# Performance work log

Hardware: AMD Instinct MI355X
Metric: run time of the kernel (lower is better)

Reference implementation:

```python
import jax, jax.numpy as jnp
import numpy as np

C = 256
DEPTH = 4
GRIDS = [(128, 128), (128, 128), (128, 128)]
B = 2
N = 32768


def _ln_c(x, g, b):
    # LayerNorm over channel dim of [B, C, N] (myLayerNorm transposes to [B,N,C])
    m = x.mean(axis=1, keepdims=True)
    v = ((x - m) ** 2).mean(axis=1, keepdims=True)
    return (x - m) * jax.lax.rsqrt(v + 1e-5) * g[None, :, None] + b[None, :, None]


def _bn_train(x, g, b):
    # BatchNorm1d (training-mode batch stats) over [B, C, L]
    m = x.mean(axis=(0, 2), keepdims=True)
    v = ((x - m) ** 2).mean(axis=(0, 2), keepdims=True)
    return (x - m) * jax.lax.rsqrt(v + 1e-5) * g[None, :, None] + b[None, :, None]


def _dwconv3(x, w, b):
    # depthwise 3x3 conv, SAME padding; x [B,C,H,W], w [C,3,3]
    out = jax.lax.conv_general_dilated(x, w[:, None, :, :], (1, 1), 'SAME',
                                       feature_group_count=C,
                                       dimension_numbers=('NCHW', 'OIHW', 'NCHW'))
    return out + b[None, :, None, None]


def setup_inputs() -> dict:
    key = jax.random.key(0)
    ks = jax.random.split(key, 20)
    tokens = jax.random.normal(ks[0], (B, C, N), jnp.float32)
    hw = GRIDS[0][0] * GRIDS[0][1]
    cell_ind = jax.random.randint(ks[1], (B, 3, N), 0, hw)
    occupied_cell = jnp.ones((B, N), jnp.float32)

    def p(k, shape, scale=0.05):
        return scale * jax.random.normal(k, shape, jnp.float32)

    inp = dict(tokens=tokens, cell_ind=cell_ind, occupied_cell=occupied_cell)
    inp['smix_ln_g'] = 1.0 + p(ks[2], (DEPTH, C))
    inp['smix_ln_b'] = p(ks[3], (DEPTH, C))
    inp['ffn_w1'] = p(ks[4], (DEPTH, C, 3, 3), 0.2)
    inp['ffn_b1'] = p(ks[5], (DEPTH, C))
    inp['ffn_w2'] = p(ks[6], (DEPTH, C, 3, 3), 0.2)
    inp['ffn_b2'] = p(ks[7], (DEPTH, C))
    inp['att_scale'] = 1.0 + p(ks[8], (DEPTH, C))
    inp['att_bn_g'] = 1.0 + p(ks[9], (DEPTH, C))
    inp['att_bn_b'] = p(ks[10], (DEPTH, C))
    inp['cmix_ln_g'] = 1.0 + p(ks[11], (DEPTH, C))
    inp['cmix_ln_b'] = p(ks[12], (DEPTH, C))
    inp['cmix_w1'] = p(ks[13], (DEPTH, C, C), 1.0 / float(np.sqrt(C)))
    inp['cmix_b1'] = p(ks[14], (DEPTH, C))
    inp['cmix_w2'] = p(ks[15], (DEPTH, C, C), 1.0 / float(np.sqrt(C)))
    inp['cmix_b2'] = p(ks[16], (DEPTH, C))
    inp['cmix_scale'] = p(ks[17], (DEPTH, C), 0.1)
    return inp


def _forward(tokens, occupied_cell, cell_ind,
             smix_ln_g, smix_ln_b, ffn_w1, ffn_b1, ffn_w2, ffn_b2,
             att_scale, att_bn_g, att_bn_b,
             cmix_ln_g, cmix_ln_b, cmix_w1, cmix_b1, cmix_w2, cmix_b2, cmix_scale):
    Bx, Cx, Nx = tokens.shape
    bidx = jnp.arange(Bx)[:, None]
    # build_proj_matrix equivalent: per-point 1/(points-in-cell) weights + clamped indices
    sp = []
    for g in range(len(GRIDS)):
        HW = GRIDS[g][0] * GRIDS[g][1]
        ci = jnp.clip(cell_ind[:, g], 0, HW - 1)
        # inflate^T @ occupied: per-cell occupied count (occupied^2 per point)
        counts = jnp.zeros((Bx, HW), tokens.dtype).at[bidx, ci].add(occupied_cell * occupied_cell)
        # inflate @ counts: per-point count of points sharing its cell
        npp = occupied_cell * jnp.take_along_axis(counts, ci, axis=1)
        sp.append((ci, occupied_cell / (npp + 1e-6)))
    skip = [jnp.zeros(GRIDS[g], tokens.dtype) for g in range(len(GRIDS))]
    for d in range(DEPTH):
        g = d % len(GRIDS)
        H, W = GRIDS[g]
        HW = H * W
        ci, wpt = sp[g]
        # --- SpatialMix ---
        r = _ln_c(tokens, smix_ln_g[d], smix_ln_b[d]) * wpt[:, None, :]
        grid = jnp.zeros((Bx, Cx, HW), tokens.dtype).at[
            jnp.arange(Bx)[:, None, None], jnp.arange(Cx)[None, :, None], ci[:, None, :]].add(r)
        grid = grid.reshape(Bx, Cx, H, W) + skip[g]
        plane = _dwconv3(jax.nn.relu(_dwconv3(grid, ffn_w1[d], ffn_b1[d])), ffn_w2[d], ffn_b2[d])
        rflat = plane.reshape(Bx, Cx, HW)
        att = jax.nn.sigmoid(_bn_train(rflat * att_scale[d][None, :, None], att_bn_g[d], att_bn_b[d]))
        rflat = att * rflat
        r = jnp.take_along_axis(rflat, jnp.broadcast_to(ci[:, None, :], (Bx, Cx, Nx)), axis=2)
        tokens = tokens + r
        skip[g] = plane
        # --- ChannelMix ---
        h = _ln_c(tokens, cmix_ln_g[d], cmix_ln_b[d])
        h = jnp.einsum('oc,bcn->bon', cmix_w1[d], h) + cmix_b1[d][None, :, None]
        h = jnp.einsum('oc,bcn->bon', cmix_w2[d], jax.nn.relu(h)) + cmix_b2[d][None, :, None]
        tokens = tokens + h * cmix_scale[d][None, :, None]
    return tokens


def reference(tokens, cell_ind, occupied_cell,
              smix_ln_g, smix_ln_b, ffn_w1, ffn_b1, ffn_w2, ffn_b2,
              att_scale, att_bn_g, att_bn_b,
              cmix_ln_g, cmix_ln_b, cmix_w1, cmix_b1, cmix_w2, cmix_b2, cmix_scale):
    return _forward(tokens, occupied_cell, cell_ind,
                    smix_ln_g, smix_ln_b, ffn_w1, ffn_b1, ffn_w2, ffn_b2,
                    att_scale, att_bn_g, att_bn_b,
                    cmix_ln_g, cmix_ln_b, cmix_w1, cmix_b1, cmix_w2, cmix_b2, cmix_scale)
```

## Files before the change

kernel.cpp:

```cpp
#include <hip/hip_runtime.h>
#include <hip/hip_bf16.h>
#include <hip/hip_fp16.h>

#define Cc 256
#define Nn 32768
#define HWc 16384
#define Bb 2

typedef float floatx4 __attribute__((ext_vector_type(4)));
typedef short bf16x8 __attribute__((ext_vector_type(8)));
typedef unsigned short ushort8v __attribute__((ext_vector_type(8)));
typedef unsigned short ushort4v __attribute__((ext_vector_type(4)));

__device__ __forceinline__ unsigned short f2b(float f){
    unsigned u = __float_as_uint(f);
    u += 0x7fff + ((u >> 16) & 1);
    return (unsigned short)(u >> 16);
}
__device__ __forceinline__ float b2f(unsigned short h){
    return __uint_as_float(((unsigned)h) << 16);
}
__device__ __forceinline__ unsigned short f2h(float f){
    return __half_as_ushort(__float2half(f));
}
__device__ __forceinline__ float h2f(unsigned short h){
    return __half2float(__ushort_as_half(h));
}

__global__ __launch_bounds__(256) void k_count(const int* __restrict__ ci,
                                               const float* __restrict__ occ,
                                               float* __restrict__ fcounts,
                                               int* __restrict__ icounts){
    int idx = blockIdx.x*256 + threadIdx.x;
    if (idx >= Bb*3*Nn) return;
    int n = idx & (Nn-1);
    int bg = idx >> 15;
    int b = bg / 3;
    int cell = min(max(ci[idx], 0), HWc-1);
    float o = occ[(b<<15) + n];
    atomicAdd(&fcounts[(bg<<14) + cell], o*o);
    atomicAdd(&icounts[(bg<<14) + cell], 1);
}

__global__ __launch_bounds__(256) void k_wpt(const int* __restrict__ ci,
                                             const float* __restrict__ occ,
                                             const float* __restrict__ fcounts,
                                             float* __restrict__ wpt){
    int idx = blockIdx.x*256 + threadIdx.x;
    if (idx >= Bb*3*Nn) return;
    int n = idx & (Nn-1);
    int bg = idx >> 15;
    int b = bg / 3;
    int cell = min(max(ci[idx], 0), HWc-1);
    float o = occ[(b<<15) + n];
    float cnt = fcounts[(bg<<14) + cell];
    wpt[idx] = o / (o*cnt + 1e-6f);
}

__global__ __launch_bounds__(256) void k_scan(const int* __restrict__ ic,
                                              int* __restrict__ starts,
                                              int* __restrict__ cursor){
    __shared__ int part[256];
    int bg = blockIdx.x;
    int t = threadIdx.x;
    const int* cs = ic + (bg << 14);
    int base = t * 64;
    int s = 0;
    for (int i = 0; i < 64; ++i) s += cs[base + i];
    part[t] = s;
    __syncthreads();
    for (int off = 1; off < 256; off <<= 1){
        int v = (t >= off) ? part[t - off] : 0;
        __syncthreads();
        part[t] += v;
        __syncthreads();
    }
    int run = (t == 0) ? 0 : part[t - 1];
    int* st = starts + bg * (HWc + 1);
    int* cu = cursor + (bg << 14);
    for (int i = 0; i < 64; ++i){
        st[base + i] = run;
        cu[base + i] = run;
        run += cs[base + i];
    }
    if (t == 255) st[HWc] = run;
}

__global__ __launch_bounds__(256) void k_fill(const int* __restrict__ ci,
                                              int* __restrict__ cursor,
                                              int* __restrict__ plist){
    int idx = blockIdx.x*256 + threadIdx.x;
    if (idx >= Bb*3*Nn) return;
    int n = idx & (Nn-1);
    int bg = idx >> 15;
    int cell = min(max(ci[idx], 0), HWc-1);
    int pos = atomicAdd(&cursor[(bg<<14) + cell], 1);
    plist[(bg<<15) + pos] = n;
}

__global__ __launch_bounds__(256) void k_wcvt(const float* __restrict__ w1,
                                              const float* __restrict__ w2,
                                              unsigned short* __restrict__ W1b,
                                              unsigned short* __restrict__ W2b){
    int idx = blockIdx.x*256 + threadIdx.x;
    if (idx >= 4*Cc*Cc) return;
    W1b[idx] = f2b(w1[idx]);
    W2b[idx] = f2b(w2[idx]);
}

__global__ __launch_bounds__(256) void k1a_ln(const float* __restrict__ tok,
                                              const float* __restrict__ wpt,
                                              const float* __restrict__ lng,
                                              const float* __restrict__ lnb,
                                              unsigned short* __restrict__ rbuf, int g){
    __shared__ float lg[Cc], lb[Cc];
    int t = threadIdx.x;
    lg[t] = lng[t];
    lb[t] = lnb[t];
    __syncthreads();
    int b = blockIdx.x >> 7;
    int p = ((blockIdx.x & 127) << 8) + t;
    const float* tb = tok + ((size_t)b << 8)*Nn + p;
    float sum = 0.f, sq = 0.f;
    for (int c = 0; c < Cc; ++c){
        float x = tb[(size_t)c << 15];
        sum += x; sq += x*x;
    }
    float m = sum * (1.f/256.f);
    float v = sq * (1.f/256.f) - m*m;
    float r = rsqrtf(fmaxf(v, 0.f) + 1e-5f);
    float wv = wpt[(b*3 + g)*Nn + p];
    unsigned short* rb = rbuf + ((size_t)((b << 15) + p) << 8);
    for (int c0 = 0; c0 < Cc; c0 += 8){
        ushort8v u;
        #pragma unroll
        for (int j = 0; j < 8; ++j){
            int c = c0 + j;
            float x = tb[(size_t)c << 15];
            float h = ((x - m)*r*lg[c] + lb[c]) * wv;
            u[j] = f2h(h);
        }
        *(ushort8v*)(rb + c0) = u;
    }
}

__global__ __launch_bounds__(256) void k1b_gather(const unsigned short* __restrict__ rbuf,
                                                  const int* __restrict__ starts,
                                                  const int* __restrict__ plist,
                                                  unsigned short* __restrict__ grid, int g){
    int t = threadIdx.x;
    int bi = blockIdx.x;
    int b = bi >> 10;
    int cell0 = (bi & 1023) << 4;
    int bg = b*3 + g;
    const int* st = starts + bg*(HWc + 1) + cell0;
    const int* pl = plist + (bg << 15);
    const unsigned short* rb = rbuf + (((size_t)b << 15) << 8);
    float acc[16];
    int s0 = st[0];
    #pragma unroll
    for (int q = 0; q < 16; ++q){
        int s1 = st[q + 1];
        float a = 0.f;
        for (int j = s0; j < s1; ++j){
            int p = pl[j];
            a += h2f(rb[((size_t)p << 8) + t]);
        }
        acc[q] = a;
        s0 = s1;
    }
    unsigned short* go = grid + ((size_t)((b << 8) + t))*HWc + cell0;
    #pragma unroll
    for (int q = 0; q < 16; q += 8){
        ushort8v u;
        #pragma unroll
        for (int j = 0; j < 8; ++j) u[j] = f2h(acc[q+j]);
        *(ushort8v*)(go + q) = u;
    }
}

__global__ __launch_bounds__(256) void k2_conv(const unsigned short* __restrict__ grid,
                                               const unsigned short* __restrict__ skip,
                                               unsigned short* __restrict__ plane,
                                               const float* __restrict__ w1, const float* __restrict__ b1,
                                               const float* __restrict__ w2, const float* __restrict__ b2,
                                               const float* __restrict__ asc,
                                               float* __restrict__ bnS, float* __restrict__ bnQ,
                                               int useskip){
    __shared__ float it[36*132];
    __shared__ float mid[34*132];
    int tid = threadIdx.x;
    int bi = blockIdx.x;
    int rt = bi & 3;
    int bc = bi >> 2;
    int c = bc & 255;
    int r0 = rt << 5;
    const unsigned short* src = grid + (size_t)bc*HWc;
    const unsigned short* sk  = skip + (size_t)bc*HWc;
    for (int i = tid; i < 36; i += 256){
        it[i*132 + 0] = 0.f; it[i*132 + 1] = 0.f;
        it[i*132 + 130] = 0.f; it[i*132 + 131] = 0.f;
    }
    for (int i = tid; i < 36*16; i += 256){
        int r = i >> 4, ch = i & 15;
        int gy = r0 - 2 + r;
        float vals[8];
        #pragma unroll
        for (int e = 0; e < 8; ++e) vals[e] = 0.f;
        if ((unsigned)gy < 128u){
            ushort8v sv = *(const ushort8v*)(src + (gy << 7) + ch*8);
            if (useskip){
                ushort8v kv = *(const ushort8v*)(sk + (gy << 7) + ch*8);
                #pragma unroll
                for (int e = 0; e < 8; ++e) vals[e] = h2f(sv[e]) + h2f(kv[e]);
            } else {
                #pragma unroll
                for (int e = 0; e < 8; ++e) vals[e] = h2f(sv[e]);
            }
        }
        #pragma unroll
        for (int e = 0; e < 8; ++e) it[r*132 + 2 + ch*8 + e] = vals[e];
    }
    float a1[9], a2[9];
    #pragma unroll
    for (int j = 0; j < 9; ++j){ a1[j] = w1[c*9+j]; a2[j] = w2[c*9+j]; }
    float bb1 = b1[c], bb2 = b2[c], sc = asc[c];
    __syncthreads();
    for (int i = tid; i < 34*130; i += 256){
        int r = i / 130, cc = i - r*130;
        int y = r0 - 1 + r, x = cc - 1;
        float v = 0.f;
        if ((unsigned)y < 128u && (unsigned)x < 128u){
            float s = 0.f;
            #pragma unroll
            for (int j = 0; j < 9; ++j) s += a1[j] * it[(r + j/3)*132 + cc + (j%3)];
            v = fmaxf(s + bb1, 0.f);
        }
        mid[r*132 + cc] = v;
    }
    __syncthreads();
    float ps = 0.f, pq = 0.f;
    unsigned short* dst = plane + (size_t)bc*HWc;
    for (int i = tid; i < 32*32; i += 256){
        int yy = i >> 5, ch = i & 31;
        int x0 = ch << 2;
        ushort4v u;
        #pragma unroll
        for (int e = 0; e < 4; ++e){
            int x = x0 + e;
            float s = 0.f;
            #pragma unroll
            for (int j = 0; j < 9; ++j) s += a2[j] * mid[(yy + j/3)*132 + x + (j%3)];
            float v = s + bb2;
            u[e] = f2h(v);
            float t = v * sc;
            ps += t; pq += t*t;
        }
        *(ushort4v*)(dst + ((r0 + yy) << 7) + x0) = u;
    }
    __syncthreads();
    it[tid] = ps; it[256 + tid] = pq;
    __syncthreads();
    for (int s2 = 128; s2 > 0; s2 >>= 1){
        if (tid < s2){ it[tid] += it[tid+s2]; it[256+tid] += it[256+tid+s2]; }
        __syncthreads();
    }
    if (tid == 0){
        atomicAdd(&bnS[c], it[0]);
        atomicAdd(&bnQ[c], it[256]);
    }
}

__global__ __launch_bounds__(256) void k3t_att_t(const unsigned short* __restrict__ plane,
                                                 const float* __restrict__ bnS, const float* __restrict__ bnQ,
                                                 const float* __restrict__ asc,
                                                 const float* __restrict__ bng, const float* __restrict__ bnb,
                                                 unsigned short* __restrict__ attp){
    __shared__ float t[32*33];
    __shared__ float P_s[32], Q_s[32];
    int tid = threadIdx.x;
    int tx = tid & 31, ty = tid >> 5;
    int bi = blockIdx.x;
    int ht = bi & 511;
    int ct = (bi >> 9) & 7;
    int b  = bi >> 12;
    int c0 = ct << 5, h0 = ht << 5;
    if (tid < 32){
        int c = c0 + tid;
        float mean = bnS[c] * (1.f/32768.f);
        float var  = bnQ[c] * (1.f/32768.f) - mean*mean;
        float inv  = rsqrtf(fmaxf(var, 0.f) + 1e-5f) * bng[c];
        P_s[tid] = asc[c] * inv;
        Q_s[tid] = bnb[c] - mean * inv;
    }
    __syncthreads();
    for (int r = ty; r < 32; r += 8){
        int c = c0 + r;
        float v = h2f(plane[(((size_t)b << 8) + c)*HWc + h0 + tx]);
        float s = 1.f / (1.f + __expf(-(P_s[r]*v + Q_s[r])));
        t[r*33 + tx] = s * v;
    }
    __syncthreads();
    for (int r = ty; r < 32; r += 8){
        attp[(((size_t)b << 14) + h0 + r)*Cc + c0 + tx] = f2h(t[tx*33 + r]);
    }
}

__global__ __launch_bounds__(512, 4) void k4_cmix(const float* __restrict__ tsrc, int tin_nc,
                                               float* __restrict__ tdst, int tout_nc,
                                               const unsigned short* __restrict__ attp,
                                               const int* __restrict__ ci,
                                               const unsigned short* __restrict__ W1,
                                               const unsigned short* __restrict__ W2,
                                               const float* __restrict__ lng, const float* __restrict__ lnb,
                                               const float* __restrict__ b1, const float* __restrict__ b2,
                                               const float* __restrict__ csc,
                                               const float* __restrict__ lng2, const float* __restrict__ lnb2,
                                               const float* __restrict__ wptb,
                                               unsigned short* __restrict__ rbufn,
                                               int g, int g2, int donext){
    __shared__ __align__(16) unsigned short hs[64*264];
    __shared__ float reds[512], redq[512];
    __shared__ float m_s[64], r_s[64];
    __shared__ int cell_s[64];
    __shared__ float lng_s[Cc], lnb_s[Cc], b1_s[Cc], b2s_s[Cc], cs_s[Cc], g2g_s[Cc], g2b_s[Cc];

    int tid = threadIdx.x;
    int bi = blockIdx.x;
    int b = bi >> 9;
    int p0 = (bi & 511) << 6;

    if (tid < 256){
        lng_s[tid] = lng[tid];
        lnb_s[tid] = lnb[tid];
        b1_s[tid]  = b1[tid];
        float cv = csc[tid];
        cs_s[tid]  = cv;
        b2s_s[tid] = b2[tid] * cv;
        g2g_s[tid] = lng2[tid];
        g2b_s[tid] = lnb2[tid];
    }
    if (tid < 64){
        int cc = ci[(b*3 + g)*Nn + p0 + tid];
        cell_s[tid] = min(max(cc, 0), HWc-1);
    }
    __syncthreads();

    int p  = tid & 63;
    int cg = tid >> 6;
    int c0 = cg << 5;

    const unsigned short* ar = attp + ((size_t)((b << 14) + cell_s[p]))*Cc + c0;
    ushort8v rr[4];
    #pragma unroll
    for (int j = 0; j < 4; ++j) rr[j] = *(const ushort8v*)(ar + 8*j);

    float vreg[32];
    float sum = 0.f, sq = 0.f;
    if (tin_nc){
        const floatx4* tn4 = (const floatx4*)(tsrc + ((((size_t)(b << 15)) + p0 + p) << 8) + c0);
        #pragma unroll
        for (int j = 0; j < 8; ++j){
            floatx4 f = tn4[j];
            #pragma unroll
            for (int e = 0; e < 4; ++e){
                int k = j*4 + e;
                float v = f[e] + h2f(rr[k >> 3][k & 7]);
                vreg[k] = v; sum += v; sq += v*v;
            }
        }
    } else {
        const float* tb = tsrc + ((size_t)b << 8)*Nn + p0 + p;
        #pragma unroll
        for (int k = 0; k < 32; ++k){
            float v = tb[(size_t)(c0 + k) << 15] + h2f(rr[k >> 3][k & 7]);
            vreg[k] = v; sum += v; sq += v*v;
        }
    }
    reds[tid] = sum; redq[tid] = sq;
    __syncthreads();
    if (tid < 64){
        float s = 0.f, q = 0.f;
        #pragma unroll
        for (int j = 0; j < 8; ++j){ s += reds[j*64 + tid]; q += redq[j*64 + tid]; }
        float m = s * (1.f/256.f);
        float var = q * (1.f/256.f) - m*m;
        m_s[tid] = m;
        r_s[tid] = rsqrtf(fmaxf(var, 0.f) + 1e-5f);
    }
    __syncthreads();
    float mp = m_s[p], rp = r_s[p];
    unsigned short* hrow = &hs[p*264 + c0];
    #pragma unroll
    for (int j = 0; j < 4; ++j){
        ushort8v u;
        #pragma unroll
        for (int e = 0; e < 8; ++e){
            int k = j*8 + e, c = c0 + k;
            u[e] = f2b((vreg[k] - mp)*rp*lng_s[c] + lnb_s[c]);
        }
        *(ushort8v*)(hrow + 8*j) = u;
    }
    __syncthreads();

    int lane = tid & 63;
    int w = tid >> 6;
    int l15 = lane & 15;
    int q4 = lane >> 4;
    floatx4 acc[2][4];
    #pragma unroll
    for (int mi = 0; mi < 2; ++mi)
        #pragma unroll
        for (int ni = 0; ni < 4; ++ni)
            acc[mi][ni] = (floatx4){0.f, 0.f, 0.f, 0.f};

    #pragma unroll
    for (int kk = 0; kk < 8; ++kk){
        int k0 = kk*32 + q4*8;
        bf16x8 bfr[4];
        #pragma unroll
        for (int ni = 0; ni < 4; ++ni)
            bfr[ni] = *(const bf16x8*)&hs[(ni*16 + l15)*264 + k0];
        #pragma unroll
        for (int mi = 0; mi < 2; ++mi){
            bf16x8 af = *(const bf16x8*)&W1[(size_t)(w*32 + mi*16 + l15)*Cc + k0];
            #pragma unroll
            for (int ni = 0; ni < 4; ++ni)
                acc[mi][ni] = __builtin_amdgcn_mfma_f32_16x16x32_bf16(af, bfr[ni], acc[mi][ni], 0, 0, 0);
        }
    }
    __syncthreads();
    #pragma unroll
    for (int mi = 0; mi < 2; ++mi)
        #pragma unroll
        for (int ni = 0; ni < 4; ++ni){
            int m0 = w*32 + mi*16 + q4*4;
            int nn = ni*16 + l15;
            ushort4v u;
            #pragma unroll
            for (int r = 0; r < 4; ++r)
                u[r] = f2b(fmaxf(acc[mi][ni][r] + b1_s[m0 + r], 0.f));
            *(ushort4v*)&hs[nn*264 + m0] = u;
        }
    __syncthreads();

    #pragma unroll
    for (int mi = 0; mi < 2; ++mi)
        #pragma unroll
        for (int ni = 0; ni < 4; ++ni)
            acc[mi][ni] = (floatx4){0.f, 0.f, 0.f, 0.f};
    #pragma unroll
    for (int kk = 0; kk < 8; ++kk){
        int k0 = kk*32 + q4*8;
        bf16x8 bfr[4];
        #pragma unroll
        for (int ni = 0; ni < 4; ++ni)
            bfr[ni] = *(const bf16x8*)&hs[(ni*16 + l15)*264 + k0];
        #pragma unroll
        for (int mi = 0; mi < 2; ++mi){
            bf16x8 af = *(const bf16x8*)&W2[(size_t)(w*32 + mi*16 + l15)*Cc + k0];
            #pragma unroll
            for (int ni = 0; ni < 4; ++ni)
                acc[mi][ni] = __builtin_amdgcn_mfma_f32_16x16x32_bf16(af, bfr[ni], acc[mi][ni], 0, 0, 0);
        }
    }
    __syncthreads();
    #pragma unroll
    for (int mi = 0; mi < 2; ++mi)
        #pragma unroll
        for (int ni = 0; ni < 4; ++ni){
            int m0 = w*32 + mi*16 + q4*4;
            int nn = ni*16 + l15;
            ushort4v u;
            #pragma unroll
            for (int r = 0; r < 4; ++r)
                u[r] = f2b(acc[mi][ni][r]*cs_s[m0 + r] + b2s_s[m0 + r]);
            *(ushort4v*)&hs[nn*264 + m0] = u;
        }
    __syncthreads();

    float sum2 = 0.f, sq2 = 0.f;
    if (tout_nc){
        float* tn = tdst + ((((size_t)(b << 15)) + p0 + p) << 8) + c0;
        #pragma unroll
        for (int j = 0; j < 4; ++j){
            ushort8v u = *(const ushort8v*)(hrow + 8*j);
            floatx4 fa, fb;
            #pragma unroll
            for (int e = 0; e < 4; ++e){
                int k = j*8 + e;
                float v = vreg[k] + b2f(u[e]);
                vreg[k] = v; fa[e] = v; sum2 += v; sq2 += v*v;
            }
            #pragma unroll
            for (int e = 4; e < 8; ++e){
                int k = j*8 + e;
                float v = vreg[k] + b2f(u[e]);
                vreg[k] = v; fb[e-4] = v; sum2 += v; sq2 += v*v;
            }
            *(floatx4*)(tn + 8*j) = fa;
            *(floatx4*)(tn + 8*j + 4) = fb;
        }
    } else {
        float* ob = tdst + ((size_t)b << 8)*Nn + p0 + p;
        #pragma unroll
        for (int j = 0; j < 4; ++j){
            ushort8v u = *(const ushort8v*)(hrow + 8*j);
            #pragma unroll
            for (int e = 0; e < 8; ++e){
                int k = j*8 + e, c = c0 + k;
                float v = vreg[k] + b2f(u[e]);
                vreg[k] = v;
                ob[(size_t)c << 15] = v;
                sum2 += v; sq2 += v*v;
            }
        }
    }
    if (donext){
        reds[tid] = sum2; redq[tid] = sq2;
        __syncthreads();
        if (tid < 64){
            float s = 0.f, q = 0.f;
            #pragma unroll
            for (int j = 0; j < 8; ++j){ s += reds[j*64 + tid]; q += redq[j*64 + tid]; }
            float m = s * (1.f/256.f);
            float var = q * (1.f/256.f) - m*m;
            m_s[tid] = m;
            r_s[tid] = rsqrtf(fmaxf(var, 0.f) + 1e-5f);
        }
        __syncthreads();
        float m2 = m_s[p], rr2 = r_s[p];
        float wv2 = wptb[(b*3 + g2)*Nn + p0 + p];
        unsigned short* rb = rbufn + ((size_t)((b << 15) + p0 + p))*Cc + c0;
        #pragma unroll
        for (int j = 0; j < 4; ++j){
            ushort8v u;
            #pragma unroll
            for (int e = 0; e < 8; ++e){
                int k = j*8 + e, c = c0 + k;
                u[e] = f2h(((vreg[k] - m2)*rr2*g2g_s[c] + g2b_s[c]) * wv2);
            }
            *(ushort8v*)(rb + 8*j) = u;
        }
    }
}

extern "C" void kernel_launch(void* const* d_in, const int* in_sizes, int n_in,
                              void* d_out, int out_size, void* d_ws, size_t ws_size,
                              hipStream_t stream){
    (void)in_sizes; (void)n_in; (void)out_size;
    const float* tokens  = (const float*)d_in[0];
    const int*   cellind = (const int*)d_in[1];
    const float* occ     = (const float*)d_in[2];
    const float* smix_g  = (const float*)d_in[3];
    const float* smix_b  = (const float*)d_in[4];
    const float* ffn_w1  = (const float*)d_in[5];
    const float* ffn_b1  = (const float*)d_in[6];
    const float* ffn_w2  = (const float*)d_in[7];
    const float* ffn_b2  = (const float*)d_in[8];
    const float* att_sc  = (const float*)d_in[9];
    const float* bn_g    = (const float*)d_in[10];
    const float* bn_b    = (const float*)d_in[11];
    const float* cm_g    = (const float*)d_in[12];
    const float* cm_b    = (const float*)d_in[13];
    const float* cw1     = (const float*)d_in[14];
    const float* cb1     = (const float*)d_in[15];
    const float* cw2     = (const float*)d_in[16];
    const float* cb2     = (const float*)d_in[17];
    const float* cscale  = (const float*)d_in[18];
    float* out = (float*)d_out;
    char* w = (char*)d_ws;

    const size_t HGRID_BYTES = (size_t)Bb*Cc*HWc*2;
    unsigned short* grid_h  = (unsigned short*)(w);
    unsigned short* attp_h  = grid_h;
    unsigned short* planeA  = (unsigned short*)(w + HGRID_BYTES);
    unsigned short* planeB  = (unsigned short*)(w + 2*HGRID_BYTES);
    unsigned short* rbuf    = (unsigned short*)(w + 3*HGRID_BYTES);
    size_t o = 3*HGRID_BYTES + (size_t)Bb*Nn*Cc*2;
    float* fcounts = (float*)(w + o); o += (size_t)Bb*3*HWc*4;
    int*   icounts = (int*)(w + o);   o += (size_t)Bb*3*HWc*4;
    float* wptb   = (float*)(w + o); o += (size_t)Bb*3*Nn*4;
    float* bnS    = (float*)(w + o);
    float* bnQ    = bnS + 256;
    o += 4096;
    unsigned short* W1b = (unsigned short*)(w + o);
    unsigned short* W2b = W1b + 4*Cc*Cc;
    o += (size_t)2*4*Cc*Cc*2;
    int* startsb  = (int*)(w + o); o += (size_t)Bb*3*(HWc+1)*4;
    int* cursors  = (int*)(w + o); o += (size_t)Bb*3*HWc*4;
    int* plistb   = (int*)(w + o); o += (size_t)Bb*3*Nn*4;
    o = (o + 255) & ~(size_t)255;
    float* tnc    = (float*)(w + o);
    size_t needed = o + (size_t)Bb*Nn*Cc*4;
    int nc_ok = (ws_size >= needed) ? 1 : 0;

    hipMemsetAsync(fcounts, 0, (size_t)2*Bb*3*HWc*4, stream);
    k_count<<<(Bb*3*Nn)/256, 256, 0, stream>>>(cellind, occ, fcounts, icounts);
    k_wpt<<<(Bb*3*Nn)/256, 256, 0, stream>>>(cellind, occ, fcounts, wptb);
    k_scan<<<Bb*3, 256, 0, stream>>>(icounts, startsb, cursors);
    k_fill<<<(Bb*3*Nn)/256, 256, 0, stream>>>(cellind, cursors, plistb);
    k_wcvt<<<(4*Cc*Cc)/256, 256, 0, stream>>>(cw1, cw2, W1b, W2b);

    k1a_ln<<<Bb*(Nn/256), 256, 0, stream>>>(tokens, wptb, smix_g, smix_b, rbuf, 0);

    for (int d = 0; d < 4; ++d){
        int g = d % 3;
        int g2 = (d + 1) % 3;
        int donext = (d < 3) ? 1 : 0;
        int useskip = (d == 3) ? 1 : 0;
        unsigned short* plane = (d == 0) ? planeA : planeB;
        int dn = (d + 1 < 4) ? d + 1 : d;

        const float* tsrc; int tin_nc;
        float* tdst; int tout_nc;
        if (nc_ok){
            tsrc = (d == 0) ? tokens : tnc;  tin_nc  = (d == 0) ? 0 : 1;
            tdst = (d == 3) ? out : tnc;     tout_nc = (d == 3) ? 0 : 1;
        } else {
            tsrc = (d == 0) ? tokens : out;  tin_nc  = 0;
            tdst = out;                      tout_nc = 0;
        }

        hipMemsetAsync(bnS, 0, 2048, stream);

        k1b_gather<<<Bb*(HWc/16), 256, 0, stream>>>(rbuf, startsb, plistb, grid_h, g);
        k2_conv<<<Bb*Cc*4, 256, 0, stream>>>(grid_h, planeA, plane,
                                             ffn_w1 + d*Cc*9, ffn_b1 + d*Cc,
                                             ffn_w2 + d*Cc*9, ffn_b2 + d*Cc,
                                             att_sc + d*Cc, bnS, bnQ, useskip);
        k3t_att_t<<<Bb*8*512, 256, 0, stream>>>(plane, bnS, bnQ, att_sc + d*Cc,
                                                bn_g + d*Cc, bn_b + d*Cc, attp_h);
        k4_cmix<<<Bb*(Nn/64), 512, 0, stream>>>(tsrc, tin_nc, tdst, tout_nc, attp_h, cellind,
                                                W1b + (size_t)d*Cc*Cc, W2b + (size_t)d*Cc*Cc,
                                                cm_g + d*Cc, cm_b + d*Cc,
                                                cb1 + d*Cc, cb2 + d*Cc, cscale + d*Cc,
                                                smix_g + dn*Cc, smix_b + dn*Cc, wptb,
                                                rbuf, g, g2, donext);
    }
}
```

Measured before the change: 753.6 us.

## Split cmix GEMMs into column halves to cut registers, raise occupancy, finer gather blocks

The channel-mix kernel now computes each of its two 256x256 GEMMs in two 32-column halves, with four accumulators instead of eight. This lowers register pressure so the launch bound can be raised from 4 to 6 blocks per CU, at the cost of extra barriers and reloading the W1/W2 fragments twice. The per-token cell index is now loaded directly into a register, which drops a shared-memory array and one barrier. The gather kernel also covers 8 cells per block instead of 16, doubling the grid to improve load balance over the variable-length point lists.

```diff
diff --git a/kernel.cpp b/kernel.cpp
--- a/kernel.cpp
+++ b/kernel.cpp
@@ -150,16 +150,16 @@
                                                   unsigned short* __restrict__ grid, int g){
     int t = threadIdx.x;
     int bi = blockIdx.x;
-    int b = bi >> 10;
-    int cell0 = (bi & 1023) << 4;
+    int b = bi >> 11;
+    int cell0 = (bi & 2047) << 3;
     int bg = b*3 + g;
     const int* st = starts + bg*(HWc + 1) + cell0;
     const int* pl = plist + (bg << 15);
     const unsigned short* rb = rbuf + (((size_t)b << 15) << 8);
-    float acc[16];
+    float acc[8];
     int s0 = st[0];
     #pragma unroll
-    for (int q = 0; q < 16; ++q){
+    for (int q = 0; q < 8; ++q){
         int s1 = st[q + 1];
         float a = 0.f;
         for (int j = s0; j < s1; ++j){
@@ -170,13 +170,10 @@
         s0 = s1;
     }
     unsigned short* go = grid + ((size_t)((b << 8) + t))*HWc + cell0;
-    #pragma unroll
-    for (int q = 0; q < 16; q += 8){
-        ushort8v u;
-        #pragma unroll
-        for (int j = 0; j < 8; ++j) u[j] = f2h(acc[q+j]);
-        *(ushort8v*)(go + q) = u;
-    }
+    ushort8v u;
+    #pragma unroll
+    for (int e = 0; e < 8; ++e) u[e] = f2h(acc[e]);
+    *(ushort8v*)go = u;
 }
 
 __global__ __launch_bounds__(256) void k2_conv(const unsigned short* __restrict__ grid,
@@ -306,7 +303,7 @@
     }
 }
 
-__global__ __launch_bounds__(512, 4) void k4_cmix(const float* __restrict__ tsrc, int tin_nc,
+__global__ __launch_bounds__(512, 6) void k4_cmix(const float* __restrict__ tsrc, int tin_nc,
                                                float* __restrict__ tdst, int tout_nc,
                                                const unsigned short* __restrict__ attp,
                                                const int* __restrict__ ci,
@@ -322,13 +319,23 @@
     __shared__ __align__(16) unsigned short hs[64*264];
     __shared__ float reds[512], redq[512];
     __shared__ float m_s[64], r_s[64];
-    __shared__ int cell_s[64];
     __shared__ float lng_s[Cc], lnb_s[Cc], b1_s[Cc], b2s_s[Cc], cs_s[Cc], g2g_s[Cc], g2b_s[Cc];
 
     int tid = threadIdx.x;
     int bi = blockIdx.x;
     int b = bi >> 9;
     int p0 = (bi & 511) << 6;
+
+    int p  = tid & 63;
+    int cg = tid >> 6;
+    int c0 = cg << 5;
+
+    int cell = ci[(b*3 + g)*Nn + p0 + p];
+    cell = min(max(cell, 0), HWc-1);
+    const unsigned short* ar = attp + ((size_t)((b << 14) + cell))*Cc + c0;
+    ushort8v rr[4];
+    #pragma unroll
+    for (int j = 0; j < 4; ++j) rr[j] = *(const ushort8v*)(ar + 8*j);
 
     if (tid < 256){
         lng_s[tid] = lng[tid];
@@ -340,20 +347,6 @@
         g2g_s[tid] = lng2[tid];
         g2b_s[tid] = lnb2[tid];
     }
-    if (tid < 64){
-        int cc = ci[(b*3 + g)*Nn + p0 + tid];
-        cell_s[tid] = min(max(cc, 0), HWc-1);
-    }
-    __syncthreads();
-
-    int p  = tid & 63;
-    int cg = tid >> 6;
-    int c0 = cg << 5;
-
-    const unsigned short* ar = attp + ((size_t)((b << 14) + cell_s[p]))*Cc + c0;
-    ushort8v rr[4];
-    #pragma unroll
-    for (int j = 0; j < 4; ++j) rr[j] = *(const ushort8v*)(ar + 8*j);
 
     float vreg[32];
     float sum = 0.f, sq = 0.f;
@@ -407,74 +400,114 @@
     int w = tid >> 6;
     int l15 = lane & 15;
     int q4 = lane >> 4;
-    floatx4 acc[2][4];
-    #pragma unroll
-    for (int mi = 0; mi < 2; ++mi)
-        #pragma unroll
-        for (int ni = 0; ni < 4; ++ni)
-            acc[mi][ni] = (floatx4){0.f, 0.f, 0.f, 0.f};
-
+    floatx4 acc[4];
+
+    #pragma unroll
+    for (int a = 0; a < 4; ++a) acc[a] = (floatx4){0.f,0.f,0.f,0.f};
     #pragma unroll
     for (int kk = 0; kk < 8; ++kk){
         int k0 = kk*32 + q4*8;
-        bf16x8 bfr[4];
-        #pragma unroll
-        for (int ni = 0; ni < 4; ++ni)
-            bfr[ni] = *(const bf16x8*)&hs[(ni*16 + l15)*264 + k0];
+        bf16x8 bfr0 = *(const bf16x8*)&hs[(l15)*264 + k0];
+        bf16x8 bfr1 = *(const bf16x8*)&hs[(16 + l15)*264 + k0];
         #pragma unroll
         for (int mi = 0; mi < 2; ++mi){
             bf16x8 af = *(const bf16x8*)&W1[(size_t)(w*32 + mi*16 + l15)*Cc + k0];
-            #pragma unroll
-            for (int ni = 0; ni < 4; ++ni)
-                acc[mi][ni] = __builtin_amdgcn_mfma_f32_16x16x32_bf16(af, bfr[ni], acc[mi][ni], 0, 0, 0);
+            acc[mi*2+0] = __builtin_amdgcn_mfma_f32_16x16x32_bf16(af, bfr0, acc[mi*2+0], 0, 0, 0);
+            acc[mi*2+1] = __builtin_amdgcn_mfma_f32_16x16x32_bf16(af, bfr1, acc[mi*2+1], 0, 0, 0);
         }
     }
     __syncthreads();
     #pragma unroll
     for (int mi = 0; mi < 2; ++mi)
         #pragma unroll
-        for (int ni = 0; ni < 4; ++ni){
+        for (int ni = 0; ni < 2; ++ni){
             int m0 = w*32 + mi*16 + q4*4;
             int nn = ni*16 + l15;
             ushort4v u;
             #pragma unroll
             for (int r = 0; r < 4; ++r)
-                u[r] = f2b(fmaxf(acc[mi][ni][r] + b1_s[m0 + r], 0.f));
+                u[r] = f2b(fmaxf(acc[mi*2+ni][r] + b1_s[m0 + r], 0.f));
             *(ushort4v*)&hs[nn*264 + m0] = u;
         }
-    __syncthreads();
-
-    #pragma unroll
-    for (int mi = 0; mi < 2; ++mi)
-        #pragma unroll
-        for (int ni = 0; ni < 4; ++ni)
-            acc[mi][ni] = (floatx4){0.f, 0.f, 0.f, 0.f};
+    #pragma unroll
+    for (int a = 0; a < 4; ++a) acc[a] = (floatx4){0.f,0.f,0.f,0.f};
     #pragma unroll
     for (int kk = 0; kk < 8; ++kk){
         int k0 = kk*32 + q4*8;
-        bf16x8 bfr[4];
-        #pragma unroll
-        for (int ni = 0; ni < 4; ++ni)
-            bfr[ni] = *(const bf16x8*)&hs[(ni*16 + l15)*264 + k0];
+        bf16x8 bfr2 = *(const bf16x8*)&hs[(32 + l15)*264 + k0];
+        bf16x8 bfr3 = *(const bf16x8*)&hs[(48 + l15)*264 + k0];
+        #pragma unroll
+        for (int mi = 0; mi < 2; ++mi){
+            bf16x8 af = *(const bf16x8*)&W1[(size_t)(w*32 + mi*16 + l15)*Cc + k0];
+            acc[mi*2+0] = __builtin_amdgcn_mfma_f32_16x16x32_bf16(af, bfr2, acc[mi*2+0], 0, 0, 0);
+            acc[mi*2+1] = __builtin_amdgcn_mfma_f32_16x16x32_bf16(af, bfr3, acc[mi*2+1], 0, 0, 0);
+        }
+    }
+    __syncthreads();
+    #pragma unroll
+    for (int mi = 0; mi < 2; ++mi)
+        #pragma unroll
+        for (int ni = 0; ni < 2; ++ni){
+            int m0 = w*32 + mi*16 + q4*4;
+            int nn = 32 + ni*16 + l15;
+            ushort4v u;
+            #pragma unroll
+            for (int r = 0; r < 4; ++r)
+                u[r] = f2b(fmaxf(acc[mi*2+ni][r] + b1_s[m0 + r], 0.f));
+            *(ushort4v*)&hs[nn*264 + m0] = u;
+        }
+    #pragma unroll
+    for (int a = 0; a < 4; ++a) acc[a] = (floatx4){0.f,0.f,0.f,0.f};
+    #pragma unroll
+    for (int kk = 0; kk < 8; ++kk){
+        int k0 = kk*32 + q4*8;
+        bf16x8 bfr0 = *(const bf16x8*)&hs[(l15)*264 + k0];
+        bf16x8 bfr1 = *(const bf16x8*)&hs[(16 + l15)*264 + k0];
         #pragma unroll
         for (int mi = 0; mi < 2; ++mi){
             bf16x8 af = *(const bf16x8*)&W2[(size_t)(w*32 + mi*16 + l15)*Cc + k0];
-            #pragma unroll
-            for (int ni = 0; ni < 4; ++ni)
-                acc[mi][ni] = __builtin_amdgcn_mfma_f32_16x16x32_bf16(af, bfr[ni], acc[mi][ni], 0, 0, 0);
+            acc[mi*2+0] = __builtin_amdgcn_mfma_f32_16x16x32_bf16(af, bfr0, acc[mi*2+0], 0, 0, 0);
+            acc[mi*2+1] = __builtin_amdgcn_mfma_f32_16x16x32_bf16(af, bfr1, acc[mi*2+1], 0, 0, 0);
         }
     }
     __syncthreads();
     #pragma unroll
     for (int mi = 0; mi < 2; ++mi)
         #pragma unroll
-        for (int ni = 0; ni < 4; ++ni){
+        for (int ni = 0; ni < 2; ++ni){
             int m0 = w*32 + mi*16 + q4*4;
             int nn = ni*16 + l15;
             ushort4v u;
             #pragma unroll
             for (int r = 0; r < 4; ++r)
-                u[r] = f2b(acc[mi][ni][r]*cs_s[m0 + r] + b2s_s[m0 + r]);
+                u[r] = f2b(acc[mi*2+ni][r]*cs_s[m0 + r] + b2s_s[m0 + r]);
+            *(ushort4v*)&hs[nn*264 + m0] = u;
+        }
+    #pragma unroll
+    for (int a = 0; a < 4; ++a) acc[a] = (floatx4){0.f,0.f,0.f,0.f};
+    #pragma unroll
+    for (int kk = 0; kk < 8; ++kk){
+        int k0 = kk*32 + q4*8;
+        bf16x8 bfr2 = *(const bf16x8*)&hs[(32 + l15)*264 + k0];
+        bf16x8 bfr3 = *(const bf16x8*)&hs[(48 + l15)*264 + k0];
+        #pragma unroll
+        for (int mi = 0; mi < 2; ++mi){
+            bf16x8 af = *(const bf16x8*)&W2[(size_t)(w*32 + mi*16 + l15)*Cc + k0];
+            acc[mi*2+0] = __builtin_amdgcn_mfma_f32_16x16x32_bf16(af, bfr2, acc[mi*2+0], 0, 0, 0);
+            acc[mi*2+1] = __builtin_amdgcn_mfma_f32_16x16x32_bf16(af, bfr3, acc[mi*2+1], 0, 0, 0);
+        }
+    }
+    __syncthreads();
+    #pragma unroll
+    for (int mi = 0; mi < 2; ++mi)
+        #pragma unroll
+        for (int ni = 0; ni < 2; ++ni){
+            int m0 = w*32 + mi*16 + q4*4;
+            int nn = 32 + ni*16 + l15;
+            ushort4v u;
+            #pragma unroll
+            for (int r = 0; r < 4; ++r)
+                u[r] = f2b(acc[mi*2+ni][r]*cs_s[m0 + r] + b2s_s[m0 + r]);
             *(ushort4v*)&hs[nn*264 + m0] = u;
         }
     __syncthreads();
@@ -624,7 +657,7 @@
 
         hipMemsetAsync(bnS, 0, 2048, stream);
 
-        k1b_gather<<<Bb*(HWc/16), 256, 0, stream>>>(rbuf, startsb, plistb, grid_h, g);
+        k1b_gather<<<Bb*(HWc/8), 256, 0, stream>>>(rbuf, startsb, plistb, grid_h, g);
         k2_conv<<<Bb*Cc*4, 256, 0, stream>>>(grid_h, planeA, plane,
                                              ffn_w1 + d*Cc*9, ffn_b1 + d*Cc,
                                              ffn_w2 + d*Cc*9, ffn_b2 + d*Cc,
```

Measured after the change: 921.4 us. 1.22x slower.
